# Kernel tuning notes

Hardware: AMD Instinct MI355X
Metric: run time of the kernel (lower is better)

## Reference

```python
import jax, jax.numpy as jnp
import numpy as np

TOP_K_POINTERS = 4


def setup_inputs() -> dict:
    key = jax.random.key(0)
    k1, k2, k3, k4 = jax.random.split(key, 4)
    B, S, IN, OUT = 2, 128, 512, 1024
    signal = jax.random.normal(k1, (B, S, IN), dtype=jnp.float32)
    phi = jax.random.normal(k2, (B, S, IN, S), dtype=jnp.float32)
    beta = jax.random.normal(k3, (B, S, IN, 1), dtype=jnp.float32)
    # nn.Linear weight: [out_features, in_features], bias=False
    W = jax.random.normal(k4, (OUT, IN), dtype=jnp.float32) * (1.0 / np.sqrt(IN))
    return {"signal": signal, "phi": phi, "beta": beta, "W": W}


def reference(signal, phi, beta, W):
    # out_signal = Linear(signal): [B,S,out]
    out_signal = jnp.einsum('bsi,oi->bso', signal, W)
    # out_beta = Linear(beta.squeeze(-1)).unsqueeze(-1): [B,S,out,1]
    out_beta = jnp.einsum('bsi,oi->bso', beta[..., 0], W)[..., None]
    # out_phi = Linear(phi.transpose(-1,-2)).transpose(-1,-2): [B,S,out,Seq]
    out_phi = jnp.einsum('bsit,oi->bsot', phi, W)
    # Causal pointer: per (b,s,o), top-k |x_i * W_oi| over in_features.
    # Chunking in the original only bounds memory; result is identical.
    contrib = jnp.abs(signal[:, :, None, :] * W[None, None, :, :])  # [B,S,out,in]
    _, idx = jax.lax.top_k(contrib, TOP_K_POINTERS)
    out_pi = idx.astype(jnp.int16)
    return out_signal, out_phi, out_beta, out_pi
```

## Files before the change

kernel.cpp:

```cpp
#include <hip/hip_runtime.h>
#include <hip/hip_bf16.h>
#include <stdint.h>

typedef __attribute__((ext_vector_type(4))) float  floatx4;
typedef __attribute__((ext_vector_type(8))) short  short8;
typedef __attribute__((ext_vector_type(4))) short  short4_t;

static constexpr int IN   = 512;
static constexpr int OUTF = 1024;
static constexpr int SEQ  = 128;

static constexpr long long OFF_SIG  = 0;
static constexpr long long OFF_PHI  = 262144;
static constexpr long long OFF_BETA = 262144LL + 33554432LL;
static constexpr long long OFF_PI   = OFF_BETA + 262144LL;

__device__ __forceinline__ unsigned short f2bf(float f) {
  union { float f; unsigned u; } x; x.f = f;
  unsigned r = x.u + 0x7fffu + ((x.u >> 16) & 1u);
  return (unsigned short)(r >> 16);
}

__device__ __forceinline__ int swz(int row, int col) {
  int g = ((row ^ (row >> 3)) & 7) << 3;
  return row * 64 + (col ^ g);
}

__global__ __launch_bounds__(512) void gemm_phi(
    const float* __restrict__ phi, const float* __restrict__ W,
    float* __restrict__ out) {
  __shared__ short lA[256 * 64];
  __shared__ short lB[128 * 64];

  int bid = blockIdx.x;
  int L   = (bid & 7) * 128 + (bid >> 3);
  int bs  = L >> 2;
  int m0  = (L & 3) * 256;

  const int tid  = threadIdx.x;
  const int lane = tid & 63;
  const int wid  = tid >> 6;
  const int wr   = wid >> 1, wc = wid & 1;

  const float* phiB = phi + (long long)bs * (IN * SEQ);
  float*       outB = out + OFF_PHI + (long long)bs * (OUTF * SEQ);

  floatx4 acc[4][4];
#pragma unroll
  for (int i = 0; i < 4; ++i)
#pragma unroll
    for (int j = 0; j < 4; ++j) acc[i][j] = floatx4{0.f, 0.f, 0.f, 0.f};

  const int tb = (tid & 31) * 4;
  const int ib = (tid >> 5) * 4;

  for (int ks = 0; ks < 8; ++ks) {
    const int i0 = ks * 64;
    __syncthreads();
#pragma unroll
    for (int r = 0; r < 4; ++r) {
      int c   = tid + 512 * r;
      int row = c >> 3, col = (c & 7) * 8;
      const float* src = W + (long long)(m0 + row) * IN + i0 + col;
      floatx4 f0 = *(const floatx4*)(src);
      floatx4 f1 = *(const floatx4*)(src + 4);
      short8 v;
      v[0] = (short)f2bf(f0[0]); v[1] = (short)f2bf(f0[1]);
      v[2] = (short)f2bf(f0[2]); v[3] = (short)f2bf(f0[3]);
      v[4] = (short)f2bf(f1[0]); v[5] = (short)f2bf(f1[1]);
      v[6] = (short)f2bf(f1[2]); v[7] = (short)f2bf(f1[3]);
      *(short8*)&lA[swz(row, col)] = v;
    }
    {
      floatx4 q[4];
#pragma unroll
      for (int j = 0; j < 4; ++j)
        q[j] = *(const floatx4*)(phiB + (long long)(i0 + ib + j) * SEQ + tb);
#pragma unroll
      for (int jj = 0; jj < 4; ++jj) {
        short4_t v;
        v[0] = (short)f2bf(q[0][jj]); v[1] = (short)f2bf(q[1][jj]);
        v[2] = (short)f2bf(q[2][jj]); v[3] = (short)f2bf(q[3][jj]);
        *(short4_t*)&lB[swz(tb + jj, ib)] = v;
      }
    }
    __syncthreads();
#pragma unroll
    for (int kk = 0; kk < 2; ++kk) {
      const int colb = kk * 32 + (lane >> 4) * 8;
      short8 af[4], bf[4];
#pragma unroll
      for (int mi = 0; mi < 4; ++mi) {
        int row = wr * 64 + mi * 16 + (lane & 15);
        af[mi] = *(const short8*)&lA[swz(row, colb)];
      }
#pragma unroll
      for (int ni = 0; ni < 4; ++ni) {
        int row = wc * 64 + ni * 16 + (lane & 15);
        bf[ni] = *(const short8*)&lB[swz(row, colb)];
      }
#pragma unroll
      for (int mi = 0; mi < 4; ++mi)
#pragma unroll
        for (int ni = 0; ni < 4; ++ni)
          acc[mi][ni] = __builtin_amdgcn_mfma_f32_16x16x32_bf16(
              af[mi], bf[ni], acc[mi][ni], 0, 0, 0);
    }
  }
#pragma unroll
  for (int mi = 0; mi < 4; ++mi)
#pragma unroll
    for (int ni = 0; ni < 4; ++ni) {
      int col = wc * 64 + ni * 16 + (lane & 15);
#pragma unroll
      for (int r = 0; r < 4; ++r) {
        int row = m0 + wr * 64 + mi * 16 + (lane >> 4) * 4 + r;
        outB[(long long)row * SEQ + col] = acc[mi][ni][r];
      }
    }
}

__global__ __launch_bounds__(256) void fused_sbp(
    const float* __restrict__ sig, const float* __restrict__ beta,
    const float* __restrict__ W, float* __restrict__ out) {
  __shared__ float ls[512], lb[512], la[512];
  const int bid = blockIdx.x;
  const int bs  = bid >> 2;
  const int oc  = bid & 3;
  const int tid = threadIdx.x;

#pragma unroll
  for (int r = 0; r < 2; ++r) {
    int i = tid + 256 * r;
    float s = sig[(long long)bs * 512 + i];
    ls[i] = s;
    la[i] = fabsf(s);
    lb[i] = beta[(long long)bs * 512 + i];
  }
  __syncthreads();

  const int o = oc * 256 + tid;
  const float* wrow = W + (long long)o * 512;
  float dsum = 0.f, bsum = 0.f;
  float tv0 = -1.f, tv1 = -1.f, tv2 = -1.f, tv3 = -1.f;
  int   ti0 = 0, ti1 = 0, ti2 = 0, ti3 = 0;

  for (int i = 0; i < 512; i += 4) {
    floatx4 w = *(const floatx4*)(wrow + i);
    floatx4 s = *(const floatx4*)(ls + i);
    floatx4 b = *(const floatx4*)(lb + i);
    floatx4 a = *(const floatx4*)(la + i);
#pragma unroll
    for (int j = 0; j < 4; ++j) {
      dsum = fmaf(s[j], w[j], dsum);
      bsum = fmaf(b[j], w[j], bsum);
      float v = fabsf(w[j]) * a[j];
      if (v > tv3) {
        int idx = i + j;
        if (v > tv0) {
          tv3 = tv2; ti3 = ti2; tv2 = tv1; ti2 = ti1; tv1 = tv0; ti1 = ti0;
          tv0 = v; ti0 = idx;
        } else if (v > tv1) {
          tv3 = tv2; ti3 = ti2; tv2 = tv1; ti2 = ti1; tv1 = v; ti1 = idx;
        } else if (v > tv2) {
          tv3 = tv2; ti3 = ti2; tv2 = v; ti2 = idx;
        } else {
          tv3 = v; ti3 = idx;
        }
      }
    }
  }

  const long long base = (long long)bs * 1024 + o;
  out[OFF_SIG + base]  = dsum;
  out[OFF_BETA + base] = bsum;
  floatx4 pv;
  pv[0] = (float)ti0; pv[1] = (float)ti1; pv[2] = (float)ti2; pv[3] = (float)ti3;
  *(floatx4*)(out + OFF_PI + base * 4) = pv;
}

extern "C" void kernel_launch(void* const* d_in, const int* in_sizes, int n_in,
                              void* d_out, int out_size, void* d_ws, size_t ws_size,
                              hipStream_t stream) {
  const float* sig  = (const float*)d_in[0];
  const float* phi  = (const float*)d_in[1];
  const float* beta = (const float*)d_in[2];
  const float* W    = (const float*)d_in[3];
  float* out = (float*)d_out;
  (void)in_sizes; (void)n_in; (void)out_size; (void)d_ws; (void)ws_size;

  hipLaunchKernelGGL(gemm_phi, dim3(1024), dim3(512), 0, stream, phi, W, out);
  hipLaunchKernelGGL(fused_sbp, dim3(1024), dim3(256), 0, stream, sig, beta, W, out);
}
```

Measured before the change: 358.9 us.

## Pre-convert W and phi to bf16 in workspace, double-buffered LDS-direct GEMM

Adds prep kernels that convert W to bf16 and transpose and convert phi to bf16 into the workspace. A new GEMM then streams both operands straight into LDS with global_load_lds, using a swizzled, double-buffered pipeline with 128x128 tiles. The aim is to take the fp32-to-bf16 conversion and the transpose out of the GEMM inner loop and to overlap loads with MFMA. In exchange it adds an extra read and a 32MB write and reread of phiT, plus two more kernel launches. It only runs when the workspace is large enough, otherwise it falls back to the old path.

After: 319.7 us. 1.12x faster.

```diff
diff --git a/kernel.cpp b/kernel.cpp
--- a/kernel.cpp
+++ b/kernel.cpp
@@ -15,10 +15,159 @@
 static constexpr long long OFF_BETA = 262144LL + 33554432LL;
 static constexpr long long OFF_PI   = OFF_BETA + 262144LL;
 
+static constexpr long long WS_WB_ELEMS   = 1024LL * 512;
+static constexpr long long WS_PHIT_ELEMS = 256LL * 128 * 512;
+static constexpr size_t    WS_NEED = (size_t)(WS_WB_ELEMS + WS_PHIT_ELEMS) * 2;
+
 __device__ __forceinline__ unsigned short f2bf(float f) {
   union { float f; unsigned u; } x; x.f = f;
   unsigned r = x.u + 0x7fffu + ((x.u >> 16) & 1u);
   return (unsigned short)(r >> 16);
+}
+
+typedef const __attribute__((address_space(1))) void* gptr_t;
+typedef __attribute__((address_space(3))) void* lptr_t;
+__device__ __forceinline__ void gl_lds16(const void* g, void* l) {
+  __builtin_amdgcn_global_load_lds((gptr_t)g, (lptr_t)l, 16, 0, 0);
+}
+
+__global__ __launch_bounds__(256) void prep_w(const float* __restrict__ W,
+                                              unsigned short* __restrict__ Wb) {
+  long long base = ((long long)blockIdx.x * 256 + threadIdx.x) * 8;
+  floatx4 f0 = *(const floatx4*)(W + base);
+  floatx4 f1 = *(const floatx4*)(W + base + 4);
+  short8 v;
+  v[0] = (short)f2bf(f0[0]); v[1] = (short)f2bf(f0[1]);
+  v[2] = (short)f2bf(f0[2]); v[3] = (short)f2bf(f0[3]);
+  v[4] = (short)f2bf(f1[0]); v[5] = (short)f2bf(f1[1]);
+  v[6] = (short)f2bf(f1[2]); v[7] = (short)f2bf(f1[3]);
+  *(short8*)(Wb + base) = v;
+}
+
+__global__ __launch_bounds__(256) void prep_phiT(const float* __restrict__ phi,
+                                                 unsigned short* __restrict__ phiT) {
+  __shared__ float lt[64 * 128];
+  const int bs = blockIdx.x >> 3;
+  const int i0 = (blockIdx.x & 7) * 64;
+  const int tid = threadIdx.x;
+  const float* src = phi + (long long)bs * (IN * SEQ) + (long long)i0 * SEQ;
+
+#pragma unroll
+  for (int r = 0; r < 8; ++r) {
+    int idx = tid + 256 * r;
+    int row = idx >> 5;
+    int colw = (idx & 31) * 4;
+    int colp = (colw + 4 * (row >> 2)) & 127;
+    *(floatx4*)&lt[row * 128 + colp] = *(const floatx4*)(src + (long long)row * SEQ + colw);
+  }
+  __syncthreads();
+
+  const int ioff = (tid & 15) * 4;
+#pragma unroll
+  for (int p = 0; p < 8; ++p) {
+    int t = p * 16 + (tid >> 4);
+    int col = (t + 4 * (tid & 15)) & 127;
+    short4_t v;
+#pragma unroll
+    for (int k = 0; k < 4; ++k) v[k] = (short)f2bf(lt[(ioff + k) * 128 + col]);
+    *(short4_t*)(phiT + ((long long)(bs * SEQ + t)) * IN + i0 + ioff) = v;
+  }
+}
+
+__global__ __launch_bounds__(256, 2) void gemm_phi2(
+    const unsigned short* __restrict__ Wb,
+    const unsigned short* __restrict__ phiT,
+    float* __restrict__ out) {
+  __shared__ unsigned short sA[2][128 * 64];
+  __shared__ unsigned short sB[2][128 * 64];
+
+  const int bid = blockIdx.x;
+  const int L   = (bid & 7) * 256 + (bid >> 3);
+  const int bs  = L >> 3;
+  const int m0  = (L & 7) * 128;
+
+  const int tid  = threadIdx.x;
+  const int lane = tid & 63;
+  const int wid  = tid >> 6;
+  const int wr   = wid >> 1, wc = wid & 1;
+
+  const unsigned short* phiB = phiT + (long long)bs * (SEQ * IN);
+  float* outB = out + OFF_PHI + (long long)bs * (OUTF * SEQ);
+
+  const int srow  = wid * 8 + (lane >> 3);
+  const int schnk = lane & 7;
+
+  floatx4 acc[4][4];
+#pragma unroll
+  for (int i = 0; i < 4; ++i)
+#pragma unroll
+    for (int j = 0; j < 4; ++j) acc[i][j] = floatx4{0.f, 0.f, 0.f, 0.f};
+
+#define STAGE(buf, kstep)                                                      \
+  {                                                                            \
+    const int i0 = (kstep) * 64;                                               \
+    _Pragma("unroll")                                                          \
+    for (int r = 0; r < 4; ++r) {                                              \
+      int row = r * 32 + srow;                                                 \
+      gl_lds16(Wb + (long long)(m0 + row) * IN + i0 + ((schnk ^ (row & 7)) << 3), \
+               &sA[buf][(r * 32 + wid * 8) * 64]);                             \
+      gl_lds16(phiB + (long long)row * IN + i0 + ((schnk ^ (row & 7)) << 3),   \
+               &sB[buf][(r * 32 + wid * 8) * 64]);                             \
+    }                                                                          \
+  }
+
+  STAGE(0, 0);
+
+  const int ra  = wr * 64 + (lane & 15);
+  const int rb  = wc * 64 + (lane & 15);
+  const int sa7 = ra & 7, sb7 = rb & 7;
+
+#pragma unroll
+  for (int k = 0; k < 8; ++k) {
+    const int cur = k & 1;
+    if (k < 7) {
+      STAGE(cur ^ 1, k + 1);
+      asm volatile("s_waitcnt vmcnt(8)" ::: "memory");
+    } else {
+      asm volatile("s_waitcnt vmcnt(0)" ::: "memory");
+    }
+    __builtin_amdgcn_s_barrier();
+    __builtin_amdgcn_sched_barrier(0);
+
+#pragma unroll
+    for (int kk = 0; kk < 2; ++kk) {
+      const int j  = kk * 4 + (lane >> 4);
+      const int ja = (j ^ sa7) << 3;
+      const int jb = (j ^ sb7) << 3;
+      short8 af[4], bv[4];
+#pragma unroll
+      for (int mi = 0; mi < 4; ++mi)
+        af[mi] = *(const short8*)&sA[cur][(ra + mi * 16) * 64 + ja];
+#pragma unroll
+      for (int ni = 0; ni < 4; ++ni)
+        bv[ni] = *(const short8*)&sB[cur][(rb + ni * 16) * 64 + jb];
+#pragma unroll
+      for (int mi = 0; mi < 4; ++mi)
+#pragma unroll
+        for (int ni = 0; ni < 4; ++ni)
+          acc[mi][ni] = __builtin_amdgcn_mfma_f32_16x16x32_bf16(
+              af[mi], bv[ni], acc[mi][ni], 0, 0, 0);
+    }
+    __builtin_amdgcn_s_barrier();
+  }
+#undef STAGE
+
+#pragma unroll
+  for (int mi = 0; mi < 4; ++mi)
+#pragma unroll
+    for (int ni = 0; ni < 4; ++ni) {
+      int t = wc * 64 + ni * 16 + (lane & 15);
+#pragma unroll
+      for (int rg = 0; rg < 4; ++rg) {
+        int o = m0 + wr * 64 + mi * 16 + (lane >> 4) * 4 + rg;
+        outB[(long long)o * SEQ + t] = acc[mi][ni][rg];
+      }
+    }
 }
 
 __device__ __forceinline__ int swz(int row, int col) {
@@ -31,29 +180,23 @@
     float* __restrict__ out) {
   __shared__ short lA[256 * 64];
   __shared__ short lB[128 * 64];
-
   int bid = blockIdx.x;
   int L   = (bid & 7) * 128 + (bid >> 3);
   int bs  = L >> 2;
   int m0  = (L & 3) * 256;
-
   const int tid  = threadIdx.x;
   const int lane = tid & 63;
   const int wid  = tid >> 6;
   const int wr   = wid >> 1, wc = wid & 1;
-
   const float* phiB = phi + (long long)bs * (IN * SEQ);
   float*       outB = out + OFF_PHI + (long long)bs * (OUTF * SEQ);
-
   floatx4 acc[4][4];
 #pragma unroll
   for (int i = 0; i < 4; ++i)
 #pragma unroll
     for (int j = 0; j < 4; ++j) acc[i][j] = floatx4{0.f, 0.f, 0.f, 0.f};
-
   const int tb = (tid & 31) * 4;
   const int ib = (tid >> 5) * 4;
-
   for (int ks = 0; ks < 8; ++ks) {
     const int i0 = ks * 64;
     __syncthreads();
@@ -187,8 +330,16 @@
   const float* beta = (const float*)d_in[2];
   const float* W    = (const float*)d_in[3];
   float* out = (float*)d_out;
-  (void)in_sizes; (void)n_in; (void)out_size; (void)d_ws; (void)ws_size;
-
-  hipLaunchKernelGGL(gemm_phi, dim3(1024), dim3(512), 0, stream, phi, W, out);
+  (void)in_sizes; (void)n_in; (void)out_size;
+
+  if (ws_size >= WS_NEED) {
+    unsigned short* Wb   = (unsigned short*)d_ws;
+    unsigned short* phiT = Wb + WS_WB_ELEMS;
+    hipLaunchKernelGGL(prep_w, dim3(256), dim3(256), 0, stream, W, Wb);
+    hipLaunchKernelGGL(prep_phiT, dim3(2048), dim3(256), 0, stream, phi, phiT);
+    hipLaunchKernelGGL(gemm_phi2, dim3(2048), dim3(256), 0, stream, Wb, phiT, out);
+  } else {
+    hipLaunchKernelGGL(gemm_phi, dim3(1024), dim3(512), 0, stream, phi, W, out);
+  }
   hipLaunchKernelGGL(fused_sbp, dim3(1024), dim3(256), 0, stream, sig, beta, W, out);
 }
```
